# Optimization experiments

Hardware: AMD Instinct MI355X
Metric: run time of the kernel (lower is better)

The kernel has to match this reference:

```python
import jax, jax.numpy as jnp
import numpy as np

B, C_IN, C_OUT, H, W = 16, 32, 32, 256, 256
M1, M2 = 32, 32  # kept Fourier modes (kbase // 2**level)


def setup_inputs() -> dict:
    key = jax.random.key(0)
    ks = jax.random.split(key, 7)
    scale = 1.0 / (C_IN * C_OUT)
    return {
        "x": jax.random.normal(ks[0], (B, C_IN, H, W), dtype=jnp.float32),
        "conv_w": jax.random.normal(ks[1], (C_OUT, 3 * C_IN), dtype=jnp.float32) * (1.0 / np.sqrt(3 * C_IN)),
        "conv_b": jax.random.normal(ks[2], (C_OUT,), dtype=jnp.float32) * 0.01,
        "w1r": jax.random.normal(ks[3], (C_IN, C_OUT, M1, M2), dtype=jnp.float32) * scale,
        "w1i": jax.random.normal(ks[4], (C_IN, C_OUT, M1, M2), dtype=jnp.float32) * scale,
        "w2r": jax.random.normal(ks[5], (C_IN, C_OUT, M1, M2), dtype=jnp.float32) * scale,
        "w2i": jax.random.normal(ks[6], (C_IN, C_OUT, M1, M2), dtype=jnp.float32) * scale,
    }


def _combi_forward(x, conv_w, conv_b, w1r, w1i, w2r, w2i):
    # ---- diff branch: EasyDiffs (x, forward-diff along H, forward-diff along W) + 1x1 conv ----
    zrow = jnp.zeros_like(x[:, :, :1, :])
    zcol = jnp.zeros_like(x[:, :, :, :1])
    dh = jnp.concatenate([x[:, :, 1:, :] - x[:, :, :-1, :], zrow], axis=2)  # [B,C,H,W]
    dw = jnp.concatenate([x[:, :, :, 1:] - x[:, :, :, :-1], zcol], axis=3)  # [B,C,H,W]
    feats = jnp.concatenate([x, dh, dw], axis=1)  # [B,3C,H,W]
    diff_out = jnp.einsum("bchw,oc->bohw", feats, conv_w) + conv_b[None, :, None, None]

    # ---- spectral branch: rfft2 -> truncated complex multiply (two corners) -> irfft2 ----
    xf = jnp.fft.rfft2(x, axes=(-2, -1))  # [B,C,H,W//2+1] complex
    w1 = w1r + 1j * w1i
    w2 = w2r + 1j * w2i
    top = jnp.einsum("bixy,ioxy->boxy", xf[:, :, :M1, :M2], w1)
    bot = jnp.einsum("bixy,ioxy->boxy", xf[:, :, -M1:, :M2], w2)
    out_ft = jnp.zeros((B, C_OUT, H, W // 2 + 1), dtype=xf.dtype)
    out_ft = out_ft.at[:, :, :M1, :M2].set(top)
    out_ft = out_ft.at[:, :, -M1:, :M2].set(bot)
    fno_out = jnp.fft.irfft2(out_ft, s=(H, W), axes=(-2, -1))

    return diff_out + fno_out


def reference(x, conv_w, conv_b, w1r, w1i, w2r, w2i):
    return _combi_forward(x, conv_w, conv_b, w1r, w1i, w2r, w2i)
```

## Files before the change

kernel.cpp:

```cpp
#include <hip/hip_runtime.h>


#define PI2_256 0.02454369260617026f

__device__ __forceinline__ unsigned short bf16r(float f) {
    unsigned u = __float_as_uint(f);
    u += 0x7fffu + ((u >> 16) & 1u);
    return (unsigned short)(u >> 16);
}
__device__ __forceinline__ float bf16tof(unsigned short h) {
    return __uint_as_float((unsigned)h << 16);
}
__device__ __forceinline__ unsigned pack2(float a, float b) {
    return (unsigned)bf16r(a) | ((unsigned)bf16r(b) << 16);
}

typedef __attribute__((ext_vector_type(8))) short short8;
typedef __attribute__((ext_vector_type(4))) float float4v;

__global__ __launch_bounds__(256) void k_twiddle(float* __restrict__ ws) {
    unsigned short* E = (unsigned short*)(ws + 8388608);
    int idx0 = blockIdx.x * 256 + threadIdx.x;
    for (int idx = idx0; idx < 4 * 64 * 72; idx += 16 * 256) {
        int c = idx / 4608;
        int rem = idx - c * 4608;
        int col = rem / 72;
        int wp = rem - col * 72;
        unsigned short hi = 0, lo = 0;
        if (wp < 64) {
            int w = c * 64 + wp;
            int ky = col & 31;
            int prod = (ky * w) & 255;
            float s, cc;
            __sincosf(PI2_256 * (float)prod, &s, &cc);
            float val = (col < 32) ? cc : -s;
            hi = bf16r(val);
            lo = bf16r(val - bf16tof(hi));
        }
        E[c * 9216 + col * 72 + wp] = hi;
        E[c * 9216 + 4608 + col * 72 + wp] = lo;
    }
}

__global__ __launch_bounds__(256) void k_tables(const float* __restrict__ cw,
                                                float* __restrict__ ws) {
    unsigned short* TWt = (unsigned short*)(ws + 6291456);
    unsigned short* CWf = (unsigned short*)(ws + 6301696);
    int id = blockIdx.x * 256 + threadIdx.x;
    int w = id >> 6, kk = id & 63;
    float s, c;
    __sincosf(PI2_256 * (float)(((kk & 31) * w) & 255), &s, &c);
    TWt[id] = bf16r(kk < 32 ? c : -s);
    if (id < 3072) {
        int j = id & 7, slot = id >> 3;
        int ks = slot >> 7, mt = (slot >> 6) & 1, lane = slot & 63;
        int m = (lane & 15) + mt * 16;
        int kb = ks * 32 + ((lane >> 4) & 3) * 8;
        CWf[id] = bf16r(cw[m * 96 + kb + j]);
    }
}

__global__ __launch_bounds__(256) void k_dftw(const float* __restrict__ x,
                                              const float* __restrict__ Ews,
                                              float* __restrict__ Ar,
                                              float* __restrict__ Ai) {
    __shared__ __align__(16) unsigned char smem[55296];
    unsigned short* Xhi = (unsigned short*)smem;
    unsigned short* Xlo = (unsigned short*)(smem + 18432);
    unsigned short* Ehi = (unsigned short*)(smem + 36864);
    float* obuf = (float*)smem;

    int t = threadIdx.x;
    int bc = blockIdx.x >> 1;
    int h0 = (blockIdx.x & 1) << 7;
    int lane = t & 63, wid = t >> 6;
    int quad = lane >> 4, col = lane & 15;

    const uint4* Ews4 = (const uint4*)Ews;

    float4v zero = {0.f, 0.f, 0.f, 0.f};
    float4v acc[4][2];
#pragma unroll
    for (int m = 0; m < 4; ++m) {
        acc[m][0] = zero;
        acc[m][1] = zero;
    }

    for (int c = 0; c < 4; ++c) {
        const float* xrow = x + ((size_t)bc * 256 + h0) * 256 + c * 64;
#pragma unroll
        for (int it = 0; it < 8; ++it) {
            int l = it * 256 + t;
            int r = l >> 4, f4 = l & 15;
            float4 v = *(const float4*)(xrow + (size_t)r * 256 + f4 * 4);
            unsigned short hx = bf16r(v.x), hy = bf16r(v.y);
            unsigned short hz = bf16r(v.z), hw = bf16r(v.w);
            unsigned hi0 = (unsigned)hx | ((unsigned)hy << 16);
            unsigned hi1 = (unsigned)hz | ((unsigned)hw << 16);
            unsigned lo0 = (unsigned)bf16r(v.x - bf16tof(hx)) |
                           ((unsigned)bf16r(v.y - bf16tof(hy)) << 16);
            unsigned lo1 = (unsigned)bf16r(v.z - bf16tof(hz)) |
                           ((unsigned)bf16r(v.w - bf16tof(hw)) << 16);
            int o = r * 72 + f4 * 4;
            *(uint2*)&Xhi[o] = make_uint2(hi0, hi1);
            *(uint2*)&Xlo[o] = make_uint2(lo0, lo1);
        }
        for (int g = t; g < 1152; g += 256)
            ((uint4*)(smem + 36864))[g] = Ews4[c * 1152 + g];
        __syncthreads();

#pragma unroll
        for (int ks = 0; ks < 2; ++ks) {
            int ko = quad * 8 + ks * 32;
            short8 ah[4], al[4], bh[2], bl[2];
#pragma unroll
            for (int m = 0; m < 4; ++m) {
                int ro = (m * 16 + col) * 72 + ko;
                ah[m] = *(const short8*)&Ehi[ro];
                al[m] = *(const short8*)&Ehi[4608 + ro];
            }
#pragma unroll
            for (int n = 0; n < 2; ++n) {
                int hr = ((wid * 2 + n) * 16 + col) * 72 + ko;
                bh[n] = *(const short8*)&Xhi[hr];
                bl[n] = *(const short8*)&Xlo[hr];
            }
#pragma unroll
            for (int m = 0; m < 4; ++m) {
#pragma unroll
                for (int n = 0; n < 2; ++n) {
                    acc[m][n] = __builtin_amdgcn_mfma_f32_16x16x32_bf16(ah[m], bh[n], acc[m][n], 0, 0, 0);
                    acc[m][n] = __builtin_amdgcn_mfma_f32_16x16x32_bf16(ah[m], bl[n], acc[m][n], 0, 0, 0);
                    acc[m][n] = __builtin_amdgcn_mfma_f32_16x16x32_bf16(al[m], bh[n], acc[m][n], 0, 0, 0);
                }
            }
        }
        __syncthreads();
    }

#pragma unroll
    for (int m = 0; m < 4; ++m) {
#pragma unroll
        for (int n = 0; n < 2; ++n) {
            int hl = (wid * 2 + n) * 16 + col;
            *(float4v*)&obuf[hl * 68 + m * 16 + quad * 4] = acc[m][n];
        }
    }
    __syncthreads();
#pragma unroll
    for (int it = 0; it < 8; ++it) {
        int l = it * 256 + t;
        int hh = l >> 4, f = l & 15;
        float4 v = *(float4*)&obuf[hh * 68 + f * 4];
        size_t g = (size_t)bc * 8192 + (size_t)(h0 + hh) * 32;
        if (f < 8) *(float4*)(Ar + g + f * 4) = v;
        else       *(float4*)(Ai + g + (f - 8) * 4) = v;
    }
}

#define DF_PITCH 72

__global__ __launch_bounds__(256) void k_dfth(const float* __restrict__ Ar,
                                              const float* __restrict__ Ai,
                                              float* __restrict__ xfr,
                                              float* __restrict__ xfi) {
    __shared__ __align__(16) unsigned short F2h[128 * DF_PITCH];
    __shared__ __align__(16) unsigned short F2l[128 * DF_PITCH];
    __shared__ __align__(16) unsigned short B2h[32 * DF_PITCH];
    __shared__ __align__(16) unsigned short B2l[32 * DF_PITCH];

    int t = threadIdx.x;
    int bc = blockIdx.x;
    int lane = t & 63, wid = t >> 6;
    int quad = lane >> 4, col = lane & 15;

    int m = t & 127;
    int kxi = m >> 1;
    int kx = (kxi < 32) ? kxi : kxi + 192;
    int neg = m & 1;
    int khalf = t >> 7;
    float c1, s1;
    __sincosf(PI2_256 * (float)kx, &s1, &c1);

    float4v zero = {0.f, 0.f, 0.f, 0.f};
    float4v acc[2][2];
    acc[0][0] = zero; acc[0][1] = zero; acc[1][0] = zero; acc[1][1] = zero;

    for (int hc = 0; hc < 8; ++hc) {
        {
            int h0 = hc * 32 + khalf * 16;
            float c, s;
            __sincosf(PI2_256 * (float)((kx * h0) & 255), &s, &c);
#pragma unroll
            for (int j = 0; j < 16; ++j) {
                int kk = 2 * (khalf * 16 + j);
                float ch = bf16tof(bf16r(c)), sh = bf16tof(bf16r(s));
                float cl = c - ch, sl = s - sh;
                unsigned hiw, low;
                if (neg == 0) { hiw = pack2(c, s);  low = pack2(cl, sl); }
                else          { hiw = pack2(-s, c); low = pack2(-sl, cl); }
                *(unsigned*)&F2h[m * DF_PITCH + kk] = hiw;
                *(unsigned*)&F2l[m * DF_PITCH + kk] = low;
                float nc = c * c1 - s * s1;
                s = s * c1 + c * s1;
                c = nc;
            }
        }
        {
            int hl = t >> 3;
            int ky0 = (t & 7) * 4;
            const float* pr = Ar + (size_t)bc * 8192 + (size_t)(hc * 32 + hl) * 32 + ky0;
            const float* pi = Ai + (size_t)bc * 8192 + (size_t)(hc * 32 + hl) * 32 + ky0;
            float4 vr = *(const float4*)pr;
            float4 vi = *(const float4*)pi;
            float fr[4] = {vr.x, vr.y, vr.z, vr.w};
            float fi[4] = {vi.x, vi.y, vi.z, vi.w};
#pragma unroll
            for (int q = 0; q < 4; ++q) {
                float ar = fr[q], ai = fi[q];
                float arh = bf16tof(bf16r(ar)), aih = bf16tof(bf16r(ai));
                *(unsigned*)&B2h[(ky0 + q) * DF_PITCH + 2 * hl] = pack2(ar, ai);
                *(unsigned*)&B2l[(ky0 + q) * DF_PITCH + 2 * hl] = pack2(ar - arh, ai - aih);
            }
        }
        __syncthreads();
#pragma unroll
        for (int ks = 0; ks < 2; ++ks) {
            int ko = ks * 32 + quad * 8;
            short8 ah[2], al[2], bh[2], bl[2];
#pragma unroll
            for (int mi = 0; mi < 2; ++mi) {
                int ro = ((wid * 2 + mi) * 16 + col) * DF_PITCH + ko;
                ah[mi] = *(const short8*)&F2h[ro];
                al[mi] = *(const short8*)&F2l[ro];
            }
#pragma unroll
            for (int ni = 0; ni < 2; ++ni) {
                int ro = (ni * 16 + col) * DF_PITCH + ko;
                bh[ni] = *(const short8*)&B2h[ro];
                bl[ni] = *(const short8*)&B2l[ro];
            }
#pragma unroll
            for (int mi = 0; mi < 2; ++mi) {
#pragma unroll
                for (int ni = 0; ni < 2; ++ni) {
                    acc[mi][ni] = __builtin_amdgcn_mfma_f32_16x16x32_bf16(ah[mi], bh[ni], acc[mi][ni], 0, 0, 0);
                    acc[mi][ni] = __builtin_amdgcn_mfma_f32_16x16x32_bf16(ah[mi], bl[ni], acc[mi][ni], 0, 0, 0);
                    acc[mi][ni] = __builtin_amdgcn_mfma_f32_16x16x32_bf16(al[mi], bh[ni], acc[mi][ni], 0, 0, 0);
                }
            }
        }
        __syncthreads();
    }
#pragma unroll
    for (int mi = 0; mi < 2; ++mi) {
#pragma unroll
        for (int ni = 0; ni < 2; ++ni) {
#pragma unroll
            for (int reg = 0; reg < 4; ++reg) {
                int mm = (wid * 2 + mi) * 16 + quad * 4 + reg;
                size_t g = (size_t)bc * 2048 + (size_t)(mm >> 1) * 32 + ni * 16 + col;
                if (mm & 1) xfi[g] = acc[mi][ni][reg];
                else        xfr[g] = acc[mi][ni][reg];
            }
        }
    }
}

__global__ __launch_bounds__(256) void k_mix(float* __restrict__ xfr,
                                             float* __restrict__ xfi,
                                             const float* __restrict__ w1r,
                                             const float* __restrict__ w1i,
                                             const float* __restrict__ w2r,
                                             const float* __restrict__ w2i) {
    __shared__ float wr[32 * 32 * 8];
    __shared__ float wi[32 * 32 * 8];
    __shared__ float xsr[32 * 8];
    __shared__ float xsi[32 * 8];
    int t = threadIdx.x;
    int kxi = (blockIdx.x >> 2) & 63;
    int ky0 = (blockIdx.x & 3) * 8;
    int b0 = (blockIdx.x >> 8) * 4;
    const float* Wr = (kxi < 32) ? w1r : w2r;
    const float* Wi = (kxi < 32) ? w1i : w2i;
    int m1 = kxi & 31;
#pragma unroll
    for (int it = 0; it < 32; ++it) {
        int l = it * 256 + t;
        int i = l >> 8, o = (l >> 3) & 31, q = l & 7;
        size_t g = (size_t)i * 32768 + (size_t)o * 1024 + m1 * 32 + ky0 + q;
        wr[l] = Wr[g];
        wi[l] = Wi[g];
    }
    __syncthreads();

    int o = t >> 3, q = t & 7;
    for (int b = b0; b < b0 + 4; ++b) {
        __syncthreads();
        {
            int i = t >> 3, qq = t & 7;
            size_t g = ((size_t)(b * 32 + i)) * 2048 + (size_t)kxi * 32 + ky0 + qq;
            xsr[t] = xfr[g];
            xsi[t] = xfi[g];
        }
        __syncthreads();
        float accr = 0.f, acci = 0.f;
#pragma unroll
        for (int i = 0; i < 32; ++i) {
            float xr = xsr[i * 8 + q], xim = xsi[i * 8 + q];
            float wrv = wr[i * 256 + o * 8 + q], wiv = wi[i * 256 + o * 8 + q];
            accr += xr * wrv - xim * wiv;
            acci += xr * wiv + xim * wrv;
        }
        size_t g = ((size_t)(b * 32 + o)) * 2048 + (size_t)kxi * 32 + ky0 + q;
        xfr[g] = accr;
        xfi[g] = acci;
    }
}

#define IF_PITCH 136

__global__ __launch_bounds__(256) void k_idfth(const float* __restrict__ ofr,
                                               const float* __restrict__ ofi,
                                               unsigned short* __restrict__ T2) {
    __shared__ __align__(16) unsigned short Fh[64 * IF_PITCH];
    __shared__ __align__(16) unsigned short Fl[64 * IF_PITCH];
    __shared__ __align__(16) unsigned short Gh[64 * IF_PITCH];
    __shared__ __align__(16) unsigned short Gl[64 * IF_PITCH];

    int t = threadIdx.x;
    int bo = blockIdx.x;
    int lane = t & 63, wid = t >> 6;
    int quad = lane >> 4, col = lane & 15;

    {
        int kxi = t >> 2;
        int ky0 = (t & 3) * 8;
        const float* pr = ofr + (size_t)bo * 2048 + (size_t)kxi * 32 + ky0;
        const float* pi = ofi + (size_t)bo * 2048 + (size_t)kxi * 32 + ky0;
        float4 r0 = *(const float4*)pr, r1 = *(const float4*)(pr + 4);
        float4 i0 = *(const float4*)pi, i1 = *(const float4*)(pi + 4);
        float fr[8] = {r0.x, r0.y, r0.z, r0.w, r1.x, r1.y, r1.z, r1.w};
        float fi[8] = {i0.x, i0.y, i0.z, i0.w, i1.x, i1.y, i1.z, i1.w};
#pragma unroll
        for (int q = 0; q < 8; ++q) {
            int ky = ky0 + q;
            float sc = ((ky == 0) ? 1.f : 2.f) * (1.f / 65536.f);
            float vr = fr[q] * sc, vi = fi[q] * sc;
            float vrh = bf16tof(bf16r(vr)), vih = bf16tof(bf16r(vi));
            float vrl = vr - vrh, vil = vi - vih;
            *(unsigned*)&Gh[ky * IF_PITCH + 2 * kxi]        = pack2(vr, -vi);
            *(unsigned*)&Gh[(32 + ky) * IF_PITCH + 2 * kxi] = pack2(vi, vr);
            *(unsigned*)&Gl[ky * IF_PITCH + 2 * kxi]        = pack2(vrl, -vil);
            *(unsigned*)&Gl[(32 + ky) * IF_PITCH + 2 * kxi] = pack2(vil, vrl);
        }
    }

    int hl_ = t & 63;
    int g = t >> 6;
    int kxi0 = g * 16;
    int kx0 = (g < 2) ? kxi0 : kxi0 + 192;

    for (int hc = 0; hc < 4; ++hc) {
        int h = hc * 64 + hl_;
        {
            float c1, s1;
            __sincosf(PI2_256 * (float)h, &s1, &c1);
            float c, s;
            __sincosf(PI2_256 * (float)((kx0 * h) & 255), &s, &c);
#pragma unroll
            for (int j = 0; j < 16; ++j) {
                int kk = 2 * (kxi0 + j);
                float ch = bf16tof(bf16r(c)), sh = bf16tof(bf16r(s));
                *(unsigned*)&Fh[hl_ * IF_PITCH + kk] = pack2(c, s);
                *(unsigned*)&Fl[hl_ * IF_PITCH + kk] = pack2(c - ch, s - sh);
                float nc = c * c1 - s * s1;
                s = s * c1 + c * s1;
                c = nc;
            }
        }
        __syncthreads();
        float4v zero = {0.f, 0.f, 0.f, 0.f};
        float4v acc[4];
        acc[0] = zero; acc[1] = zero; acc[2] = zero; acc[3] = zero;
#pragma unroll
        for (int ks = 0; ks < 4; ++ks) {
            int ko = ks * 32 + quad * 8;
            short8 bh = *(const short8*)&Gh[(wid * 16 + col) * IF_PITCH + ko];
            short8 bl = *(const short8*)&Gl[(wid * 16 + col) * IF_PITCH + ko];
#pragma unroll
            for (int mt = 0; mt < 4; ++mt) {
                int ro = (mt * 16 + col) * IF_PITCH + ko;
                short8 ah = *(const short8*)&Fh[ro];
                short8 al = *(const short8*)&Fl[ro];
                acc[mt] = __builtin_amdgcn_mfma_f32_16x16x32_bf16(ah, bh, acc[mt], 0, 0, 0);
                acc[mt] = __builtin_amdgcn_mfma_f32_16x16x32_bf16(ah, bl, acc[mt], 0, 0, 0);
                acc[mt] = __builtin_amdgcn_mfma_f32_16x16x32_bf16(al, bh, acc[mt], 0, 0, 0);
            }
        }
        unsigned short* dst = T2 + (size_t)bo * 16384 + (size_t)hc * 64 * 64;
        int n = wid * 16 + col;
#pragma unroll
        for (int mt = 0; mt < 4; ++mt) {
#pragma unroll
            for (int reg = 0; reg < 4; ++reg) {
                int hh = mt * 16 + quad * 4 + reg;
                dst[hh * 64 + n] = bf16r(acc[mt][reg]);
            }
        }
        __syncthreads();
    }
}

__global__ __launch_bounds__(256, 4) void k_final(const float* __restrict__ x,
                                                  const unsigned short* __restrict__ cwf,
                                                  const unsigned short* __restrict__ TWt,
                                                  const float* __restrict__ cb,
                                                  const unsigned short* __restrict__ T2,
                                                  float* __restrict__ out) {
    __shared__ __align__(16) unsigned short Bf[5 * 8 * 64 * 8];

    int t = threadIdx.x;
    int b = blockIdx.x >> 9;
    int h = (blockIdx.x >> 1) & 255;
    int w0 = (blockIdx.x & 1) << 7;
    int lane = t & 63, wid = t >> 6;
    int quad = lane >> 4, col = lane & 15;

    short8 a[5][2];
#pragma unroll
    for (int ks = 0; ks < 3; ++ks)
#pragma unroll
        for (int mt = 0; mt < 2; ++mt)
            a[ks][mt] = *(const short8*)&cwf[((ks * 2 + mt) * 64 + lane) * 8];
#pragma unroll
    for (int ks = 3; ks < 5; ++ks)
#pragma unroll
        for (int mt = 0; mt < 2; ++mt) {
            int m = (lane & 15) + mt * 16;
            a[ks][mt] = *(const short8*)&T2[((size_t)(b * 32 + m) * 256 + h) * 64
                                            + (ks - 3) * 32 + quad * 8];
        }

    int nn = t & 127, half = t >> 7;
    int w = w0 + nn;
    int wt = nn >> 4, colw = nn & 15;
    int hs = (h < 255) ? h + 1 : h;
    int we = (w < 255) ? 1 : 0;
#pragma unroll
    for (int ip = 0; ip < 2; ++ip) {
        int i0 = half * 16 + ip * 8;
        float c[8], sv[8], ev[8];
#pragma unroll
        for (int j = 0; j < 8; ++j) {
            const float* xp = x + ((size_t)(b * 32 + i0 + j)) * 65536;
            c[j]  = xp[h * 256 + w];
            sv[j] = xp[hs * 256 + w];
            ev[j] = xp[h * 256 + w + we];
        }
        uint4 pc, ps, pe;
        pc.x = pack2(c[0], c[1]); pc.y = pack2(c[2], c[3]);
        pc.z = pack2(c[4], c[5]); pc.w = pack2(c[6], c[7]);
        ps.x = pack2(sv[0] - c[0], sv[1] - c[1]); ps.y = pack2(sv[2] - c[2], sv[3] - c[3]);
        ps.z = pack2(sv[4] - c[4], sv[5] - c[5]); ps.w = pack2(sv[6] - c[6], sv[7] - c[7]);
        pe.x = pack2(ev[0] - c[0], ev[1] - c[1]); pe.y = pack2(ev[2] - c[2], ev[3] - c[3]);
        pe.z = pack2(ev[4] - c[4], ev[5] - c[5]); pe.w = pack2(ev[6] - c[6], ev[7] - c[7]);
        int qp = half * 2 + ip;
        *(uint4*)&Bf[((0 * 8 + wt) * 64 + qp * 16 + colw) * 8] = pc;
        *(uint4*)&Bf[((1 * 8 + wt) * 64 + qp * 16 + colw) * 8] = ps;
        *(uint4*)&Bf[((2 * 8 + wt) * 64 + qp * 16 + colw) * 8] = pe;
    }
    {
        const uint4* tw = (const uint4*)&TWt[w * 64 + half * 32];
#pragma unroll
        for (int q = 0; q < 4; ++q) {
            uint4 v = tw[q];
            *(uint4*)&Bf[(((3 + half) * 8 + wt) * 64 + q * 16 + colw) * 8] = v;
        }
    }
    __syncthreads();

    float4v zero = {0.f, 0.f, 0.f, 0.f};
    float4v acc[2][2];
    acc[0][0] = zero; acc[0][1] = zero; acc[1][0] = zero; acc[1][1] = zero;
#pragma unroll
    for (int ks = 0; ks < 5; ++ks) {
#pragma unroll
        for (int nt = 0; nt < 2; ++nt) {
            short8 ub = *(const short8*)&Bf[((ks * 8 + wid * 2 + nt) * 64 + lane) * 8];
            acc[0][nt] = __builtin_amdgcn_mfma_f32_16x16x32_bf16(a[ks][0], ub, acc[0][nt], 0, 0, 0);
            acc[1][nt] = __builtin_amdgcn_mfma_f32_16x16x32_bf16(a[ks][1], ub, acc[1][nt], 0, 0, 0);
        }
    }

#pragma unroll
    for (int mt = 0; mt < 2; ++mt) {
#pragma unroll
        for (int nt = 0; nt < 2; ++nt) {
#pragma unroll
            for (int reg = 0; reg < 4; ++reg) {
                int o = mt * 16 + quad * 4 + reg;
                int ww = w0 + wid * 32 + nt * 16 + col;
                out[(((size_t)(b * 32 + o)) * 256 + h) * 256 + ww] = acc[mt][nt][reg] + cb[o];
            }
        }
    }
}

extern "C" void kernel_launch(void* const* d_in, const int* in_sizes, int n_in,
                              void* d_out, int out_size, void* d_ws, size_t ws_size,
                              hipStream_t stream) {
    const float* x = (const float*)d_in[0];
    const float* conv_w = (const float*)d_in[1];
    const float* conv_b = (const float*)d_in[2];
    const float* w1r = (const float*)d_in[3];
    const float* w1i = (const float*)d_in[4];
    const float* w2r = (const float*)d_in[5];
    const float* w2i = (const float*)d_in[6];
    float* out = (float*)d_out;

    float* ws = (float*)d_ws;
    float* Ar = ws;
    float* Ai = ws + 4194304;
    unsigned short* T2 = (unsigned short*)ws;
    float* xfr = ws + 8388608;
    float* xfi = ws + 9437184;
    const float* Ews = ws + 8388608;
    const unsigned short* TWt = (const unsigned short*)(ws + 6291456);
    const unsigned short* CWf = (const unsigned short*)(ws + 6301696);

    k_twiddle<<<16, 256, 0, stream>>>(ws);
    k_dftw<<<1024, 256, 0, stream>>>(x, Ews, Ar, Ai);
    k_dfth<<<512, 256, 0, stream>>>(Ar, Ai, xfr, xfi);
    k_tables<<<64, 256, 0, stream>>>(conv_w, ws);
    k_mix<<<1024, 256, 0, stream>>>(xfr, xfi, w1r, w1i, w2r, w2i);
    k_idfth<<<512, 256, 0, stream>>>(xfr, xfi, T2);
    k_final<<<8192, 256, 0, stream>>>(x, CWf, TWt, conv_b, T2, out);
}
```

Baseline: 427.9 us.

## Load MFMA operands directly from global, dropping LDS staging in DFT and final kernels

```diff
diff --git a/kernel.cpp b/kernel.cpp
--- a/kernel.cpp
+++ b/kernel.cpp
@@ -60,15 +60,11 @@
     }
 }
 
-__global__ __launch_bounds__(256) void k_dftw(const float* __restrict__ x,
-                                              const float* __restrict__ Ews,
-                                              float* __restrict__ Ar,
-                                              float* __restrict__ Ai) {
-    __shared__ __align__(16) unsigned char smem[55296];
-    unsigned short* Xhi = (unsigned short*)smem;
-    unsigned short* Xlo = (unsigned short*)(smem + 18432);
-    unsigned short* Ehi = (unsigned short*)(smem + 36864);
-    float* obuf = (float*)smem;
+__global__ __launch_bounds__(256, 4) void k_dftw(const float* __restrict__ x,
+                                                 const float* __restrict__ Ews,
+                                                 float* __restrict__ Ar,
+                                                 float* __restrict__ Ai) {
+    __shared__ __align__(16) float obuf[128 * 68];
 
     int t = threadIdx.x;
     int bc = blockIdx.x >> 1;
@@ -76,7 +72,7 @@
     int lane = t & 63, wid = t >> 6;
     int quad = lane >> 4, col = lane & 15;
 
-    const uint4* Ews4 = (const uint4*)Ews;
+    const unsigned short* EH = (const unsigned short*)Ews;
 
     float4v zero = {0.f, 0.f, 0.f, 0.f};
     float4v acc[4][2];
@@ -86,44 +82,38 @@
         acc[m][1] = zero;
     }
 
+    const float* xbase = x + ((size_t)bc * 256 + h0) * 256;
+
     for (int c = 0; c < 4; ++c) {
-        const float* xrow = x + ((size_t)bc * 256 + h0) * 256 + c * 64;
-#pragma unroll
-        for (int it = 0; it < 8; ++it) {
-            int l = it * 256 + t;
-            int r = l >> 4, f4 = l & 15;
-            float4 v = *(const float4*)(xrow + (size_t)r * 256 + f4 * 4);
-            unsigned short hx = bf16r(v.x), hy = bf16r(v.y);
-            unsigned short hz = bf16r(v.z), hw = bf16r(v.w);
-            unsigned hi0 = (unsigned)hx | ((unsigned)hy << 16);
-            unsigned hi1 = (unsigned)hz | ((unsigned)hw << 16);
-            unsigned lo0 = (unsigned)bf16r(v.x - bf16tof(hx)) |
-                           ((unsigned)bf16r(v.y - bf16tof(hy)) << 16);
-            unsigned lo1 = (unsigned)bf16r(v.z - bf16tof(hz)) |
-                           ((unsigned)bf16r(v.w - bf16tof(hw)) << 16);
-            int o = r * 72 + f4 * 4;
-            *(uint2*)&Xhi[o] = make_uint2(hi0, hi1);
-            *(uint2*)&Xlo[o] = make_uint2(lo0, lo1);
-        }
-        for (int g = t; g < 1152; g += 256)
-            ((uint4*)(smem + 36864))[g] = Ews4[c * 1152 + g];
-        __syncthreads();
-
+        const unsigned short* Ec = EH + c * 9216;
 #pragma unroll
         for (int ks = 0; ks < 2; ++ks) {
-            int ko = quad * 8 + ks * 32;
-            short8 ah[4], al[4], bh[2], bl[2];
+            int ko = ks * 32 + quad * 8;
+            short8 ah[4], al[4];
 #pragma unroll
             for (int m = 0; m < 4; ++m) {
                 int ro = (m * 16 + col) * 72 + ko;
-                ah[m] = *(const short8*)&Ehi[ro];
-                al[m] = *(const short8*)&Ehi[4608 + ro];
-            }
+                ah[m] = *(const short8*)&Ec[ro];
+                al[m] = *(const short8*)&Ec[4608 + ro];
+            }
+            short8 bh[2], bl[2];
 #pragma unroll
             for (int n = 0; n < 2; ++n) {
-                int hr = ((wid * 2 + n) * 16 + col) * 72 + ko;
-                bh[n] = *(const short8*)&Xhi[hr];
-                bl[n] = *(const short8*)&Xlo[hr];
+                int row = (wid * 2 + n) * 16 + col;
+                const float* xp = xbase + (size_t)row * 256 + c * 64 + ko;
+                float4 v0 = *(const float4*)xp;
+                float4 v1 = *(const float4*)(xp + 4);
+                float v[8] = {v0.x, v0.y, v0.z, v0.w, v1.x, v1.y, v1.z, v1.w};
+                union { uint4 u; short8 s; } ph, pl;
+                ph.u.x = pack2(v[0], v[1]); ph.u.y = pack2(v[2], v[3]);
+                ph.u.z = pack2(v[4], v[5]); ph.u.w = pack2(v[6], v[7]);
+                float r[8];
+#pragma unroll
+                for (int j = 0; j < 8; ++j) r[j] = v[j] - bf16tof(bf16r(v[j]));
+                pl.u.x = pack2(r[0], r[1]); pl.u.y = pack2(r[2], r[3]);
+                pl.u.z = pack2(r[4], r[5]); pl.u.w = pack2(r[6], r[7]);
+                bh[n] = ph.s;
+                bl[n] = pl.s;
             }
 #pragma unroll
             for (int m = 0; m < 4; ++m) {
@@ -135,7 +125,6 @@
                 }
             }
         }
-        __syncthreads();
     }
 
 #pragma unroll
@@ -412,13 +401,13 @@
     }
 }
 
-__global__ __launch_bounds__(256, 4) void k_final(const float* __restrict__ x,
+__global__ __launch_bounds__(256, 5) void k_final(const float* __restrict__ x,
                                                   const unsigned short* __restrict__ cwf,
                                                   const unsigned short* __restrict__ TWt,
                                                   const float* __restrict__ cb,
                                                   const unsigned short* __restrict__ T2,
                                                   float* __restrict__ out) {
-    __shared__ __align__(16) unsigned short Bf[5 * 8 * 64 * 8];
+    __shared__ __align__(16) unsigned short Bf[3 * 8 * 64 * 8];
 
     int t = threadIdx.x;
     int b = blockIdx.x >> 9;
@@ -427,6 +416,37 @@
     int lane = t & 63, wid = t >> 6;
     int quad = lane >> 4, col = lane & 15;
 
+    {
+        int nn = t & 127, half = t >> 7;
+        int w = w0 + nn;
+        int wt = nn >> 4, colw = nn & 15;
+        int hs = (h < 255) ? h + 1 : h;
+        int we = (w < 255) ? 1 : 0;
+#pragma unroll
+        for (int ip = 0; ip < 2; ++ip) {
+            int i0 = half * 16 + ip * 8;
+            float c[8], sv[8], ev[8];
+#pragma unroll
+            for (int j = 0; j < 8; ++j) {
+                const float* xp = x + ((size_t)(b * 32 + i0 + j)) * 65536;
+                c[j]  = xp[h * 256 + w];
+                sv[j] = xp[hs * 256 + w];
+                ev[j] = xp[h * 256 + w + we];
+            }
+            uint4 pc, ps, pe;
+            pc.x = pack2(c[0], c[1]); pc.y = pack2(c[2], c[3]);
+            pc.z = pack2(c[4], c[5]); pc.w = pack2(c[6], c[7]);
+            ps.x = pack2(sv[0] - c[0], sv[1] - c[1]); ps.y = pack2(sv[2] - c[2], sv[3] - c[3]);
+            ps.z = pack2(sv[4] - c[4], sv[5] - c[5]); ps.w = pack2(sv[6] - c[6], sv[7] - c[7]);
+            pe.x = pack2(ev[0] - c[0], ev[1] - c[1]); pe.y = pack2(ev[2] - c[2], ev[3] - c[3]);
+            pe.z = pack2(ev[4] - c[4], ev[5] - c[5]); pe.w = pack2(ev[6] - c[6], ev[7] - c[7]);
+            int qp = half * 2 + ip;
+            *(uint4*)&Bf[((0 * 8 + wt) * 64 + qp * 16 + colw) * 8] = pc;
+            *(uint4*)&Bf[((1 * 8 + wt) * 64 + qp * 16 + colw) * 8] = ps;
+            *(uint4*)&Bf[((2 * 8 + wt) * 64 + qp * 16 + colw) * 8] = pe;
+        }
+    }
+
     short8 a[5][2];
 #pragma unroll
     for (int ks = 0; ks < 3; ++ks)
@@ -441,55 +461,34 @@
             a[ks][mt] = *(const short8*)&T2[((size_t)(b * 32 + m) * 256 + h) * 64
                                             + (ks - 3) * 32 + quad * 8];
         }
-
-    int nn = t & 127, half = t >> 7;
-    int w = w0 + nn;
-    int wt = nn >> 4, colw = nn & 15;
-    int hs = (h < 255) ? h + 1 : h;
-    int we = (w < 255) ? 1 : 0;
-#pragma unroll
-    for (int ip = 0; ip < 2; ++ip) {
-        int i0 = half * 16 + ip * 8;
-        float c[8], sv[8], ev[8];
-#pragma unroll
-        for (int j = 0; j < 8; ++j) {
-            const float* xp = x + ((size_t)(b * 32 + i0 + j)) * 65536;
-            c[j]  = xp[h * 256 + w];
-            sv[j] = xp[hs * 256 + w];
-            ev[j] = xp[h * 256 + w + we];
-        }
-        uint4 pc, ps, pe;
-        pc.x = pack2(c[0], c[1]); pc.y = pack2(c[2], c[3]);
-        pc.z = pack2(c[4], c[5]); pc.w = pack2(c[6], c[7]);
-        ps.x = pack2(sv[0] - c[0], sv[1] - c[1]); ps.y = pack2(sv[2] - c[2], sv[3] - c[3]);
-        ps.z = pack2(sv[4] - c[4], sv[5] - c[5]); ps.w = pack2(sv[6] - c[6], sv[7] - c[7]);
-        pe.x = pack2(ev[0] - c[0], ev[1] - c[1]); pe.y = pack2(ev[2] - c[2], ev[3] - c[3]);
-        pe.z = pack2(ev[4] - c[4], ev[5] - c[5]); pe.w = pack2(ev[6] - c[6], ev[7] - c[7]);
-        int qp = half * 2 + ip;
-        *(uint4*)&Bf[((0 * 8 + wt) * 64 + qp * 16 + colw) * 8] = pc;
-        *(uint4*)&Bf[((1 * 8 + wt) * 64 + qp * 16 + colw) * 8] = ps;
-        *(uint4*)&Bf[((2 * 8 + wt) * 64 + qp * 16 + colw) * 8] = pe;
-    }
-    {
-        const uint4* tw = (const uint4*)&TWt[w * 64 + half * 32];
-#pragma unroll
-        for (int q = 0; q < 4; ++q) {
-            uint4 v = tw[q];
-            *(uint4*)&Bf[(((3 + half) * 8 + wt) * 64 + q * 16 + colw) * 8] = v;
-        }
-    }
+    short8 twf[2][2];
+#pragma unroll
+    for (int ks2 = 0; ks2 < 2; ++ks2)
+#pragma unroll
+        for (int nt = 0; nt < 2; ++nt) {
+            int w = w0 + wid * 32 + nt * 16 + col;
+            twf[ks2][nt] = *(const short8*)&TWt[w * 64 + ks2 * 32 + quad * 8];
+        }
     __syncthreads();
 
     float4v zero = {0.f, 0.f, 0.f, 0.f};
     float4v acc[2][2];
     acc[0][0] = zero; acc[0][1] = zero; acc[1][0] = zero; acc[1][1] = zero;
 #pragma unroll
-    for (int ks = 0; ks < 5; ++ks) {
+    for (int ks = 0; ks < 3; ++ks) {
 #pragma unroll
         for (int nt = 0; nt < 2; ++nt) {
             short8 ub = *(const short8*)&Bf[((ks * 8 + wid * 2 + nt) * 64 + lane) * 8];
             acc[0][nt] = __builtin_amdgcn_mfma_f32_16x16x32_bf16(a[ks][0], ub, acc[0][nt], 0, 0, 0);
             acc[1][nt] = __builtin_amdgcn_mfma_f32_16x16x32_bf16(a[ks][1], ub, acc[1][nt], 0, 0, 0);
+        }
+    }
+#pragma unroll
+    for (int ks2 = 0; ks2 < 2; ++ks2) {
+#pragma unroll
+        for (int nt = 0; nt < 2; ++nt) {
+            acc[0][nt] = __builtin_amdgcn_mfma_f32_16x16x32_bf16(a[3 + ks2][0], twf[ks2][nt], acc[0][nt], 0, 0, 0);
+            acc[1][nt] = __builtin_amdgcn_mfma_f32_16x16x32_bf16(a[3 + ks2][1], twf[ks2][nt], acc[1][nt], 0, 0, 0);
         }
     }
 
```

Result: no change. 428.3 us (+0.1%).
